# Performance work log

Measured on AMD Instinct MI355X. Metric: run time of the kernel, lower is better.

## Reference

```python
import jax, jax.numpy as jnp
import numpy as np

HIDDEN_DIM = 1024
SEQ_LEN = 4096
D_IN = 1024


def setup_inputs() -> dict:
    key = jax.random.key(0)
    ks = jax.random.split(key, 9)
    s = 1.0 / np.sqrt(D_IN)
    return {
        "q": jax.random.normal(ks[0], (SEQ_LEN, D_IN), jnp.float32),
        "k": jax.random.normal(ks[1], (SEQ_LEN, D_IN), jnp.float32),
        "v": jax.random.normal(ks[2], (SEQ_LEN, D_IN), jnp.float32),
        "Wq": jax.random.normal(ks[3], (D_IN, HIDDEN_DIM), jnp.float32) * s,
        "bq": jnp.zeros((HIDDEN_DIM,), jnp.float32),
        "Wk": jax.random.normal(ks[4], (D_IN, HIDDEN_DIM), jnp.float32) * s,
        "bk": jnp.zeros((HIDDEN_DIM,), jnp.float32),
        "Wv": jax.random.normal(ks[5], (D_IN, HIDDEN_DIM), jnp.float32) * s,
        "bv": jnpp_zeros() if False else jnp.zeros((HIDDEN_DIM,), jnp.float32),
    }


def reference(q, k, v, Wq, bq, Wk, bk, Wv, bv):
    # Dense projections (flax Dense: x @ W + b)
    query = q @ Wq + bq          # [S, H]
    key_p = k @ Wk + bk          # [S, H]
    value = v @ Wv + bv          # [S, H]
    # scores = Q K^T / sqrt(hidden_dim)  -> [S, S]
    scores = jnp.matmul(query, key_p.T) / jnp.sqrt(jnp.float32(HIDDEN_DIM))
    weights = jax.nn.softmax(scores, axis=-1)
    context = jnp.matmul(weights, value)  # [S, H]
    return context
```

## Files before the change

kernel.cpp:

```cpp
#include <hip/hip_runtime.h>


typedef short short4v __attribute__((ext_vector_type(4)));
typedef short short8  __attribute__((ext_vector_type(8)));
typedef float f32x4   __attribute__((ext_vector_type(4)));

#define MFMA16 __builtin_amdgcn_mfma_f32_16x16x32_bf16

__device__ __forceinline__ short f2bf(float f) {
    union { float f; unsigned u; } x; x.f = f;
    unsigned r = (x.u + 0x7FFFu + ((x.u >> 16) & 1u)) >> 16;
    return (short)r;
}
__device__ __forceinline__ float bf2f(short s) {
    union { unsigned u; float f; } x;
    x.u = ((unsigned)(unsigned short)s) << 16; return x.f;
}
__device__ __forceinline__ void store_out(short* p, float v) { *p = f2bf(v); }
__device__ __forceinline__ void store_out(float* p, float v) { *p = v; }

__device__ __forceinline__ void gl2lds(const short* g, short* l) {
    __builtin_amdgcn_global_load_lds(
        (const __attribute__((address_space(1))) void*)g,
        (__attribute__((address_space(3))) void*)l, 16, 0, 0);
}

__global__ __launch_bounds__(256) void prep_w(
    const float* __restrict__ W0, const float* __restrict__ W1,
    const float* __restrict__ W2, short* __restrict__ Wt)
{
    __shared__ float tile[64][65];
    const float* W = blockIdx.z == 0 ? W0 : (blockIdx.z == 1 ? W1 : W2);
    short* T = Wt + (size_t)blockIdx.z * 1048576;
    const int c0 = blockIdx.x * 64;
    const int r0 = blockIdx.y * 64;
    const int tx = threadIdx.x & 63;
    const int ty = threadIdx.x >> 6;
    #pragma unroll
    for (int p = 0; p < 16; ++p) {
        int r = ty + p * 4;
        tile[r][tx] = W[(size_t)(r0 + r) * 1024 + c0 + tx];
    }
    __syncthreads();
    #pragma unroll
    for (int p = 0; p < 16; ++p) {
        int r = ty + p * 4;
        T[(size_t)(c0 + r) * 1024 + r0 + tx] = f2bf(tile[tx][r]);
    }
}

__global__ __launch_bounds__(256) void cast_qkv(
    const float* __restrict__ q, const float* __restrict__ k,
    const float* __restrict__ v, short* __restrict__ xb)
{
    const float* src = blockIdx.z == 0 ? q : (blockIdx.z == 1 ? k : v);
    short* dst = xb + (size_t)blockIdx.z * 4194304;
    for (int i = blockIdx.x * 256 + threadIdx.x; i < 1048576; i += 256 * 1024) {
        float4 f = ((const float4*)src)[i];
        short4v o;
        o[0] = f2bf(f.x); o[1] = f2bf(f.y); o[2] = f2bf(f.z); o[3] = f2bf(f.w);
        ((short4v*)dst)[i] = o;
    }
}

__global__ __launch_bounds__(256) void transpose_v(
    const short* __restrict__ src, short* __restrict__ dst)
{
    __shared__ short t[64][65];
    const int c0 = blockIdx.x * 64;
    const int r0 = blockIdx.y * 64;
    const int tx = threadIdx.x & 63;
    const int ty = threadIdx.x >> 6;
    #pragma unroll
    for (int p = 0; p < 16; ++p) {
        const int r = p * 4 + ty;
        t[r][tx] = src[(size_t)(r0 + r) * 1024 + c0 + tx];
    }
    __syncthreads();
    #pragma unroll
    for (int p = 0; p < 16; ++p) {
        const int r = p * 4 + ty;
        dst[(size_t)(c0 + r) * 4096 + r0 + tx] = t[tx][r];
    }
}

template <typename TOut, int MODE>
__global__ __launch_bounds__(512, 4) void gemm128(
    const short* __restrict__ A, const short* __restrict__ Bt,
    const float* __restrict__ b0, const float* __restrict__ b1,
    const float* __restrict__ b2,
    TOut* __restrict__ C, float* __restrict__ P1, float* __restrict__ P2,
    float* __restrict__ P3,
    int M, int N, int lda, int ldb, float scale,
    int nc, int nc_last, int kstep)
{
    __shared__ short Lds[24576];

    const int t    = threadIdx.x;
    const int lane = t & 63;
    const int wv   = t >> 6;

    const int nb  = gridDim.x;
    const int bid = blockIdx.y * nb + blockIdx.x;
    const int band   = bid / (8 * nb);
    const int within = bid - band * 8 * nb;
    const int m0 = (band * 8 + (within & 7)) * 128;
    const int n0 = (within >> 3) * 256;

    const float* bias = nullptr;
    int kbeg = 0;
    TOut* Cw = C;
    if constexpr (MODE == 1) {
        const int z = blockIdx.z;
        A  += (size_t)z * M * lda;
        Bt += (size_t)z * N * ldb;
        Cw  = C + (size_t)z * M * N;
        bias = z == 0 ? b0 : (z == 1 ? b1 : b2);
    }
    if constexpr (MODE == 2) {
        const int z = blockIdx.z;
        kbeg = z * kstep;
        if (z == (int)gridDim.z - 1) nc = nc_last;
        Cw = (TOut*)(z == 0 ? (float*)C : (z == 1 ? P1 : (z == 2 ? P2 : P3)));
    }
    (void)b0; (void)b1; (void)b2; (void)P1; (void)P2; (void)P3;
    (void)nc_last; (void)kstep;

    const int srow = lane >> 2;
    const int skof = ((lane & 3) ^ ((lane >> 3) & 3)) * 8;
    const short* pA  = A  + (size_t)(m0 + wv * 16 + srow) * lda + kbeg + skof;
    const short* pB0 = Bt + (size_t)(n0 + wv * 16 + srow) * ldb + kbeg + skof;
    const short* pB1 = pB0 + (size_t)128 * ldb;
    short* sA  = Lds + wv * 512;
    short* sB0 = Lds + 4096 + wv * 512;
    short* sB1 = Lds + 8192 + wv * 512;

    const int wm = wv >> 2, wn = wv & 3;
    const int lr = lane & 15, lq = lane >> 4;
    const int pcol = lq ^ ((lr >> 1) & 3);
    const short* rdA = Lds + (wm * 64 + lr) * 32 + pcol * 8;
    const short* rdB = Lds + 4096 + (wn * 64 + lr) * 32 + pcol * 8;

    f32x4 acc[4][4];
    #pragma unroll
    for (int i = 0; i < 4; ++i)
        #pragma unroll
        for (int j = 0; j < 4; ++j) { f32x4 z4 = {0.f,0.f,0.f,0.f}; acc[i][j] = z4; }

#define STAGE(c) {                                                        \
    const int s_ = (c) & 1;                                               \
    const size_t ko_ = (size_t)(c) * 32;                                  \
    gl2lds(pA  + ko_, sA  + s_ * 12288);                                  \
    gl2lds(pB0 + ko_, sB0 + s_ * 12288);                                  \
    gl2lds(pB1 + ko_, sB1 + s_ * 12288); }

#define COMPUTE(c) {                                                      \
    const short* rA_ = rdA + ((c) & 1) * 12288;                           \
    const short* rB_ = rdB + ((c) & 1) * 12288;                           \
    short8 af[4], bf_[4];                                                 \
    _Pragma("unroll") for (int i = 0; i < 4; ++i)                         \
        af[i] = *(const short8*)(rA_ + i * 512);                          \
    _Pragma("unroll") for (int j = 0; j < 4; ++j)                         \
        bf_[j] = *(const short8*)(rB_ + j * 512);                         \
    __builtin_amdgcn_s_setprio(1);                                        \
    _Pragma("unroll") for (int i = 0; i < 4; ++i)                         \
        _Pragma("unroll") for (int j = 0; j < 4; ++j)                     \
            acc[i][j] = MFMA16(af[i], bf_[j], acc[i][j], 0, 0, 0);        \
    __builtin_amdgcn_s_setprio(0); }

    STAGE(0);

    for (int c = 0; c < nc - 1; ++c) {
        STAGE(c + 1);
        asm volatile("s_waitcnt vmcnt(3)" ::: "memory");
        __builtin_amdgcn_s_barrier();
        COMPUTE(c);
        __builtin_amdgcn_s_barrier();
    }
    asm volatile("s_waitcnt vmcnt(0)" ::: "memory");
    __builtin_amdgcn_s_barrier();
    COMPUTE(nc - 1);
#undef COMPUTE
#undef STAGE

    #pragma unroll
    for (int i = 0; i < 4; ++i) {
        const int crow = m0 + wm * 64 + i * 16 + lq * 4;
        #pragma unroll
        for (int j = 0; j < 4; ++j) {
            const int ccol = n0 + wn * 64 + j * 16 + lr;
            float bb = 0.f;
            if constexpr (MODE == 1) bb = bias[ccol];
            #pragma unroll
            for (int r = 0; r < 4; ++r) {
                float val = acc[i][j][r] * scale + bb;
                store_out(&Cw[(size_t)(crow + r) * N + ccol], val);
            }
        }
    }
}

__global__ __launch_bounds__(256) void softmax_bf16(short* __restrict__ S)
{
    const int row = blockIdx.x;
    short8* r8 = (short8*)(S + (size_t)row * 4096);
    const int t = threadIdx.x;

    float x[16];
    #pragma unroll
    for (int i = 0; i < 2; ++i) {
        short8 raw = r8[t + 256 * i];
        #pragma unroll
        for (int j = 0; j < 8; ++j) x[8 * i + j] = bf2f(raw[j]);
    }
    float m = -1e30f;
    #pragma unroll
    for (int i = 0; i < 16; ++i) m = fmaxf(m, x[i]);
    #pragma unroll
    for (int off = 32; off > 0; off >>= 1) m = fmaxf(m, __shfl_xor(m, off));

    __shared__ float redm[4], reds[4];
    const int wv = t >> 6;
    if ((t & 63) == 0) redm[wv] = m;
    __syncthreads();
    m = fmaxf(fmaxf(redm[0], redm[1]), fmaxf(redm[2], redm[3]));

    float s = 0.f;
    #pragma unroll
    for (int i = 0; i < 16; ++i) { x[i] = __expf(x[i] - m); s += x[i]; }
    #pragma unroll
    for (int off = 32; off > 0; off >>= 1) s += __shfl_xor(s, off);
    if ((t & 63) == 0) reds[wv] = s;
    __syncthreads();
    s = reds[0] + reds[1] + reds[2] + reds[3];
    const float inv = 1.f / s;

    #pragma unroll
    for (int i = 0; i < 2; ++i) {
        short8 o;
        #pragma unroll
        for (int j = 0; j < 8; ++j) o[j] = f2bf(x[8 * i + j] * inv);
        r8[t + 256 * i] = o;
    }
}

__global__ __launch_bounds__(256) void combine(
    float* __restrict__ out, const float* __restrict__ a,
    const float* __restrict__ b, const float* __restrict__ c, int np)
{
    for (int i = blockIdx.x * 256 + threadIdx.x; i < 1048576; i += 256 * 1024) {
        float4 o = ((const float4*)out)[i];
        float4 x = ((const float4*)a)[i];
        float4 y = ((const float4*)b)[i];
        o.x += x.x + y.x; o.y += x.y + y.y;
        o.z += x.z + y.z; o.w += x.w + y.w;
        if (np == 3) {
            float4 w = ((const float4*)c)[i];
            o.x += w.x; o.y += w.y; o.z += w.z; o.w += w.w;
        }
        ((float4*)out)[i] = o;
    }
}

extern "C" void kernel_launch(void* const* d_in, const int* in_sizes, int n_in,
                              void* d_out, int out_size, void* d_ws, size_t ws_size,
                              hipStream_t stream)
{
    const float* q  = (const float*)d_in[0];
    const float* k  = (const float*)d_in[1];
    const float* v  = (const float*)d_in[2];
    const float* Wq = (const float*)d_in[3];
    const float* bq = (const float*)d_in[4];
    const float* Wk = (const float*)d_in[5];
    const float* bk = (const float*)d_in[6];
    const float* Wv = (const float*)d_in[7];
    const float* bv = (const float*)d_in[8];
    float* out = (float*)d_out;

    char* ws = (char*)d_ws;
    const size_t MB = 1ull << 20;
    short* Wt = (short*)(ws + 0);
    short* xb = (short*)(ws + 6 * MB);
    short* pr = (short*)(ws + 30 * MB);
    short* S  = (short*)(ws + 46 * MB);
    short* Vt = (short*)(ws + 78 * MB);
    float* p1 = (float*)(ws + 0);
    float* p2 = (float*)(ws + 16 * MB);
    float* p3 = (float*)(ws + 86 * MB);
    const int SK = (ws_size >= 102 * MB) ? 4 : 3;

    prep_w<<<dim3(16, 16, 3), 256, 0, stream>>>(Wq, Wk, Wv, Wt);
    cast_qkv<<<dim3(1024, 1, 3), 256, 0, stream>>>(q, k, v, xb);
    gemm128<short, 1><<<dim3(4, 32, 3), 512, 0, stream>>>(
        xb, Wt, bq, bk, bv, pr, nullptr, nullptr, nullptr,
        4096, 1024, 1024, 1024, 1.f, 32, 32, 0);
    transpose_v<<<dim3(16, 64), 256, 0, stream>>>(pr + 8 * 1024 * 1024, Vt);
    gemm128<short, 0><<<dim3(16, 32), 512, 0, stream>>>(
        pr, pr + 4 * 1024 * 1024, nullptr, nullptr, nullptr, S,
        nullptr, nullptr, nullptr,
        4096, 4096, 1024, 1024, 0.03125f, 32, 32, 0);
    softmax_bf16<<<4096, 256, 0, stream>>>(S);
    if (SK == 4) {
        gemm128<float, 2><<<dim3(4, 32, 4), 512, 0, stream>>>(
            S, Vt, nullptr, nullptr, nullptr, out, p1, p2, p3,
            4096, 1024, 4096, 4096, 1.f, 32, 32, 1024);
        combine<<<1024, 256, 0, stream>>>(out, p1, p2, p3, 3);
    } else {
        gemm128<float, 2><<<dim3(4, 32, 3), 512, 0, stream>>>(
            S, Vt, nullptr, nullptr, nullptr, out, p1, p2, nullptr,
            4096, 1024, 4096, 4096, 1.f, 42, 44, 1344);
        combine<<<1024, 256, 0, stream>>>(out, p1, p2, nullptr, 2);
    }
}
```

Before: 254.2 us.

## Fuse V transpose into projection GEMM epilogue and shrink GEMM tile to 128x128

Removes the separate transpose_v kernel: the V-projection blocks write their bf16 output transposed directly into Vt through LDS staging in the epilogue. All GEMMs switch from 512-thread 128x256 tiles to 256-thread 128x128 tiles with doubled grids. This is meant to cut one launch and one round trip of V through memory, and to improve load balance across CUs. The cost is lower data reuse per block and an extra LDS pass in the V epilogue.

```diff
diff --git a/kernel.cpp b/kernel.cpp
--- a/kernel.cpp
+++ b/kernel.cpp
@@ -63,38 +63,17 @@
     }
 }
 
-__global__ __launch_bounds__(256) void transpose_v(
-    const short* __restrict__ src, short* __restrict__ dst)
-{
-    __shared__ short t[64][65];
-    const int c0 = blockIdx.x * 64;
-    const int r0 = blockIdx.y * 64;
-    const int tx = threadIdx.x & 63;
-    const int ty = threadIdx.x >> 6;
-    #pragma unroll
-    for (int p = 0; p < 16; ++p) {
-        const int r = p * 4 + ty;
-        t[r][tx] = src[(size_t)(r0 + r) * 1024 + c0 + tx];
-    }
-    __syncthreads();
-    #pragma unroll
-    for (int p = 0; p < 16; ++p) {
-        const int r = p * 4 + ty;
-        dst[(size_t)(c0 + r) * 4096 + r0 + tx] = t[tx][r];
-    }
-}
-
 template <typename TOut, int MODE>
-__global__ __launch_bounds__(512, 4) void gemm128(
+__global__ __launch_bounds__(256, 4) void gemm128(
     const short* __restrict__ A, const short* __restrict__ Bt,
     const float* __restrict__ b0, const float* __restrict__ b1,
     const float* __restrict__ b2,
     TOut* __restrict__ C, float* __restrict__ P1, float* __restrict__ P2,
-    float* __restrict__ P3,
+    float* __restrict__ P3, short* __restrict__ Vt,
     int M, int N, int lda, int ldb, float scale,
     int nc, int nc_last, int kstep)
 {
-    __shared__ short Lds[24576];
+    __shared__ short Lds[16384];
 
     const int t    = threadIdx.x;
     const int lane = t & 63;
@@ -105,7 +84,7 @@
     const int band   = bid / (8 * nb);
     const int within = bid - band * 8 * nb;
     const int m0 = (band * 8 + (within & 7)) * 128;
-    const int n0 = (within >> 3) * 256;
+    const int n0 = (within >> 3) * 128;
 
     const float* bias = nullptr;
     int kbeg = 0;
@@ -123,19 +102,21 @@
         if (z == (int)gridDim.z - 1) nc = nc_last;
         Cw = (TOut*)(z == 0 ? (float*)C : (z == 1 ? P1 : (z == 2 ? P2 : P3)));
     }
-    (void)b0; (void)b1; (void)b2; (void)P1; (void)P2; (void)P3;
+    (void)b0; (void)b1; (void)b2; (void)P1; (void)P2; (void)P3; (void)Vt;
     (void)nc_last; (void)kstep;
 
     const int srow = lane >> 2;
     const int skof = ((lane & 3) ^ ((lane >> 3) & 3)) * 8;
-    const short* pA  = A  + (size_t)(m0 + wv * 16 + srow) * lda + kbeg + skof;
-    const short* pB0 = Bt + (size_t)(n0 + wv * 16 + srow) * ldb + kbeg + skof;
-    const short* pB1 = pB0 + (size_t)128 * ldb;
-    short* sA  = Lds + wv * 512;
-    short* sB0 = Lds + 4096 + wv * 512;
-    short* sB1 = Lds + 8192 + wv * 512;
-
-    const int wm = wv >> 2, wn = wv & 3;
+    const short* pA0 = A  + (size_t)(m0 + wv * 32 + srow) * lda + kbeg + skof;
+    const short* pA1 = pA0 + (size_t)16 * lda;
+    const short* pB0 = Bt + (size_t)(n0 + wv * 32 + srow) * ldb + kbeg + skof;
+    const short* pB1 = pB0 + (size_t)16 * ldb;
+    short* sA0 = Lds + wv * 1024;
+    short* sA1 = sA0 + 512;
+    short* sB0 = Lds + 4096 + wv * 1024;
+    short* sB1 = sB0 + 512;
+
+    const int wm = wv >> 1, wn = wv & 1;
     const int lr = lane & 15, lq = lane >> 4;
     const int pcol = lq ^ ((lr >> 1) & 3);
     const short* rdA = Lds + (wm * 64 + lr) * 32 + pcol * 8;
@@ -150,13 +131,14 @@
 #define STAGE(c) {                                                        \
     const int s_ = (c) & 1;                                               \
     const size_t ko_ = (size_t)(c) * 32;                                  \
-    gl2lds(pA  + ko_, sA  + s_ * 12288);                                  \
-    gl2lds(pB0 + ko_, sB0 + s_ * 12288);                                  \
-    gl2lds(pB1 + ko_, sB1 + s_ * 12288); }
+    gl2lds(pA0 + ko_, sA0 + s_ * 8192);                                   \
+    gl2lds(pA1 + ko_, sA1 + s_ * 8192);                                   \
+    gl2lds(pB0 + ko_, sB0 + s_ * 8192);                                   \
+    gl2lds(pB1 + ko_, sB1 + s_ * 8192); }
 
 #define COMPUTE(c) {                                                      \
-    const short* rA_ = rdA + ((c) & 1) * 12288;                           \
-    const short* rB_ = rdB + ((c) & 1) * 12288;                           \
+    const short* rA_ = rdA + ((c) & 1) * 8192;                            \
+    const short* rB_ = rdB + ((c) & 1) * 8192;                            \
     short8 af[4], bf_[4];                                                 \
     _Pragma("unroll") for (int i = 0; i < 4; ++i)                         \
         af[i] = *(const short8*)(rA_ + i * 512);                          \
@@ -172,7 +154,7 @@
 
     for (int c = 0; c < nc - 1; ++c) {
         STAGE(c + 1);
-        asm volatile("s_waitcnt vmcnt(3)" ::: "memory");
+        asm volatile("s_waitcnt vmcnt(4)" ::: "memory");
         __builtin_amdgcn_s_barrier();
         COMPUTE(c);
         __builtin_amdgcn_s_barrier();
@@ -183,6 +165,39 @@
 #undef COMPUTE
 #undef STAGE
 
+    if constexpr (MODE == 1) {
+        if (blockIdx.z == 2) {
+            #pragma unroll
+            for (int hh = 0; hh < 2; ++hh) {
+                __syncthreads();
+                if (wn == hh) {
+                    #pragma unroll
+                    for (int i = 0; i < 4; ++i) {
+                        #pragma unroll
+                        for (int j = 0; j < 4; ++j) {
+                            const int colL = wn * 64 + j * 16 + lr;
+                            const float bb = bias[n0 + colL];
+                            #pragma unroll
+                            for (int r = 0; r < 4; ++r) {
+                                const int rowL = wm * 64 + i * 16 + lq * 4 + r;
+                                Lds[(colL - 64 * hh) * 136 + rowL] =
+                                    f2bf(acc[i][j][r] * scale + bb);
+                            }
+                        }
+                    }
+                }
+                __syncthreads();
+                const int c = t >> 2, part = t & 3;
+                short* dst = Vt + (size_t)(n0 + 64 * hh + c) * 4096
+                                + m0 + part * 32;
+                const short* src = &Lds[c * 136 + part * 32];
+                #pragma unroll
+                for (int s = 0; s < 4; ++s)
+                    ((short8*)dst)[s] = ((const short8*)src)[s];
+            }
+            return;
+        }
+    }
     #pragma unroll
     for (int i = 0; i < 4; ++i) {
         const int crow = m0 + wm * 64 + i * 16 + lq * 4;
@@ -291,23 +306,22 @@
 
     prep_w<<<dim3(16, 16, 3), 256, 0, stream>>>(Wq, Wk, Wv, Wt);
     cast_qkv<<<dim3(1024, 1, 3), 256, 0, stream>>>(q, k, v, xb);
-    gemm128<short, 1><<<dim3(4, 32, 3), 512, 0, stream>>>(
-        xb, Wt, bq, bk, bv, pr, nullptr, nullptr, nullptr,
+    gemm128<short, 1><<<dim3(8, 32, 3), 256, 0, stream>>>(
+        xb, Wt, bq, bk, bv, pr, nullptr, nullptr, nullptr, Vt,
         4096, 1024, 1024, 1024, 1.f, 32, 32, 0);
-    transpose_v<<<dim3(16, 64), 256, 0, stream>>>(pr + 8 * 1024 * 1024, Vt);
-    gemm128<short, 0><<<dim3(16, 32), 512, 0, stream>>>(
+    gemm128<short, 0><<<dim3(32, 32), 256, 0, stream>>>(
         pr, pr + 4 * 1024 * 1024, nullptr, nullptr, nullptr, S,
-        nullptr, nullptr, nullptr,
+        nullptr, nullptr, nullptr, nullptr,
         4096, 4096, 1024, 1024, 0.03125f, 32, 32, 0);
     softmax_bf16<<<4096, 256, 0, stream>>>(S);
     if (SK == 4) {
-        gemm128<float, 2><<<dim3(4, 32, 4), 512, 0, stream>>>(
-            S, Vt, nullptr, nullptr, nullptr, out, p1, p2, p3,
+        gemm128<float, 2><<<dim3(8, 32, 4), 256, 0, stream>>>(
+            S, Vt, nullptr, nullptr, nullptr, out, p1, p2, p3, nullptr,
             4096, 1024, 4096, 4096, 1.f, 32, 32, 1024);
         combine<<<1024, 256, 0, stream>>>(out, p1, p2, p3, 3);
     } else {
-        gemm128<float, 2><<<dim3(4, 32, 3), 512, 0, stream>>>(
-            S, Vt, nullptr, nullptr, nullptr, out, p1, p2, nullptr,
+        gemm128<float, 2><<<dim3(8, 32, 3), 256, 0, stream>>>(
+            S, Vt, nullptr, nullptr, nullptr, out, p1, p2, nullptr, nullptr,
             4096, 1024, 4096, 4096, 1.f, 42, 44, 1344);
         combine<<<1024, 256, 0, stream>>>(out, p1, p2, nullptr, 2);
     }
```

Measured after the change: 263.0 us. 1.03x slower.

## Fuse V transpose into projection GEMM epilogue and stage bf16 stores through LDS

Applied to the files above, without the earlier changes.

The projection GEMM's V slice now writes its output transposed directly into Vt through an LDS staging tile, which removes the separate transpose_v kernel and its extra pass over V. The bf16 epilogues for the projection and QK^T GEMMs also stage tiles in LDS so each thread writes 16-byte vectors, replacing scattered 2-byte stores. The cost is extra barriers and LDS traffic in the epilogue, plus reuse of the GEMM's LDS buffer after the main loop.

```diff
diff --git a/kernel.cpp b/kernel.cpp
--- a/kernel.cpp
+++ b/kernel.cpp
@@ -16,8 +16,6 @@
     union { unsigned u; float f; } x;
     x.u = ((unsigned)(unsigned short)s) << 16; return x.f;
 }
-__device__ __forceinline__ void store_out(short* p, float v) { *p = f2bf(v); }
-__device__ __forceinline__ void store_out(float* p, float v) { *p = v; }
 
 __device__ __forceinline__ void gl2lds(const short* g, short* l) {
     __builtin_amdgcn_global_load_lds(
@@ -63,34 +61,13 @@
     }
 }
 
-__global__ __launch_bounds__(256) void transpose_v(
-    const short* __restrict__ src, short* __restrict__ dst)
-{
-    __shared__ short t[64][65];
-    const int c0 = blockIdx.x * 64;
-    const int r0 = blockIdx.y * 64;
-    const int tx = threadIdx.x & 63;
-    const int ty = threadIdx.x >> 6;
-    #pragma unroll
-    for (int p = 0; p < 16; ++p) {
-        const int r = p * 4 + ty;
-        t[r][tx] = src[(size_t)(r0 + r) * 1024 + c0 + tx];
-    }
-    __syncthreads();
-    #pragma unroll
-    for (int p = 0; p < 16; ++p) {
-        const int r = p * 4 + ty;
-        dst[(size_t)(c0 + r) * 4096 + r0 + tx] = t[tx][r];
-    }
-}
-
 template <typename TOut, int MODE>
 __global__ __launch_bounds__(512, 4) void gemm128(
     const short* __restrict__ A, const short* __restrict__ Bt,
     const float* __restrict__ b0, const float* __restrict__ b1,
     const float* __restrict__ b2,
     TOut* __restrict__ C, float* __restrict__ P1, float* __restrict__ P2,
-    float* __restrict__ P3,
+    float* __restrict__ P3, short* __restrict__ Vt,
     int M, int N, int lda, int ldb, float scale,
     int nc, int nc_last, int kstep)
 {
@@ -114,7 +91,7 @@
         const int z = blockIdx.z;
         A  += (size_t)z * M * lda;
         Bt += (size_t)z * N * ldb;
-        Cw  = C + (size_t)z * M * N;
+        Cw  = C + (size_t)(z < 2 ? z : 0) * M * N;
         bias = z == 0 ? b0 : (z == 1 ? b1 : b2);
     }
     if constexpr (MODE == 2) {
@@ -123,7 +100,7 @@
         if (z == (int)gridDim.z - 1) nc = nc_last;
         Cw = (TOut*)(z == 0 ? (float*)C : (z == 1 ? P1 : (z == 2 ? P2 : P3)));
     }
-    (void)b0; (void)b1; (void)b2; (void)P1; (void)P2; (void)P3;
+    (void)b0; (void)b1; (void)b2; (void)P1; (void)P2; (void)P3; (void)Vt;
     (void)nc_last; (void)kstep;
 
     const int srow = lane >> 2;
@@ -183,19 +160,81 @@
 #undef COMPUTE
 #undef STAGE
 
+    if constexpr (MODE == 1) {
+        if (blockIdx.z == 2) {
+            #pragma unroll
+            for (int hh = 0; hh < 4; ++hh) {
+                __syncthreads();
+                if (wn == hh) {
+                    #pragma unroll
+                    for (int i = 0; i < 4; ++i) {
+                        #pragma unroll
+                        for (int j = 0; j < 4; ++j) {
+                            const int colL = j * 16 + lr;
+                            const float bb = bias[n0 + hh * 64 + colL];
+                            #pragma unroll
+                            for (int r = 0; r < 4; ++r) {
+                                const int rowL = wm * 64 + i * 16 + lq * 4 + r;
+                                Lds[colL * 136 + rowL] =
+                                    f2bf(acc[i][j][r] * scale + bb);
+                            }
+                        }
+                    }
+                }
+                __syncthreads();
+                const int c = t >> 3, part = t & 7;
+                short* dst = Vt + (size_t)(n0 + hh * 64 + c) * 4096
+                                + m0 + part * 16;
+                const short* src = &Lds[c * 136 + part * 16];
+                *(short8*)dst       = *(const short8*)src;
+                *(short8*)(dst + 8) = *(const short8*)(src + 8);
+            }
+            return;
+        }
+    }
+
+    if constexpr (sizeof(TOut) == 2) {
+        #pragma unroll
+        for (int p = 0; p < 2; ++p) {
+            __syncthreads();
+            if (wm == p) {
+                #pragma unroll
+                for (int i = 0; i < 4; ++i) {
+                    #pragma unroll
+                    for (int j = 0; j < 4; ++j) {
+                        const int col = wn * 64 + j * 16 + lr;
+                        float bb = 0.f;
+                        if constexpr (MODE == 1) bb = bias[n0 + col];
+                        #pragma unroll
+                        for (int r = 0; r < 4; ++r) {
+                            const int row = i * 16 + lq * 4 + r;
+                            Lds[row * 272 + col] =
+                                f2bf(acc[i][j][r] * scale + bb);
+                        }
+                    }
+                }
+            }
+            __syncthreads();
+            const int row = t >> 3, part = t & 7;
+            short* dst = (short*)Cw + (size_t)(m0 + p * 64 + row) * N
+                          + n0 + part * 32;
+            const short* src = &Lds[row * 272 + part * 32];
+            #pragma unroll
+            for (int s = 0; s < 4; ++s)
+                ((short8*)dst)[s] = ((const short8*)src)[s];
+        }
+        return;
+    }
+
     #pragma unroll
     for (int i = 0; i < 4; ++i) {
         const int crow = m0 + wm * 64 + i * 16 + lq * 4;
         #pragma unroll
         for (int j = 0; j < 4; ++j) {
             const int ccol = n0 + wn * 64 + j * 16 + lr;
-            float bb = 0.f;
-            if constexpr (MODE == 1) bb = bias[ccol];
             #pragma unroll
-            for (int r = 0; r < 4; ++r) {
-                float val = acc[i][j][r] * scale + bb;
-                store_out(&Cw[(size_t)(crow + r) * N + ccol], val);
-            }
+            for (int r = 0; r < 4; ++r)
+                Cw[(size_t)(crow + r) * N + ccol] = acc[i][j][r] * scale;
         }
     }
 }
@@ -292,22 +331,21 @@
     prep_w<<<dim3(16, 16, 3), 256, 0, stream>>>(Wq, Wk, Wv, Wt);
     cast_qkv<<<dim3(1024, 1, 3), 256, 0, stream>>>(q, k, v, xb);
     gemm128<short, 1><<<dim3(4, 32, 3), 512, 0, stream>>>(
-        xb, Wt, bq, bk, bv, pr, nullptr, nullptr, nullptr,
+        xb, Wt, bq, bk, bv, pr, nullptr, nullptr, nullptr, Vt,
         4096, 1024, 1024, 1024, 1.f, 32, 32, 0);
-    transpose_v<<<dim3(16, 64), 256, 0, stream>>>(pr + 8 * 1024 * 1024, Vt);
     gemm128<short, 0><<<dim3(16, 32), 512, 0, stream>>>(
         pr, pr + 4 * 1024 * 1024, nullptr, nullptr, nullptr, S,
-        nullptr, nullptr, nullptr,
+        nullptr, nullptr, nullptr, nullptr,
         4096, 4096, 1024, 1024, 0.03125f, 32, 32, 0);
     softmax_bf16<<<4096, 256, 0, stream>>>(S);
     if (SK == 4) {
         gemm128<float, 2><<<dim3(4, 32, 4), 512, 0, stream>>>(
-            S, Vt, nullptr, nullptr, nullptr, out, p1, p2, p3,
+            S, Vt, nullptr, nullptr, nullptr, out, p1, p2, p3, nullptr,
             4096, 1024, 4096, 4096, 1.f, 32, 32, 1024);
         combine<<<1024, 256, 0, stream>>>(out, p1, p2, p3, 3);
     } else {
         gemm128<float, 2><<<dim3(4, 32, 3), 512, 0, stream>>>(
-            S, Vt, nullptr, nullptr, nullptr, out, p1, p2, nullptr,
+            S, Vt, nullptr, nullptr, nullptr, out, p1, p2, nullptr, nullptr,
             4096, 1024, 4096, 4096, 1.f, 42, 44, 1344);
         combine<<<1024, 256, 0, stream>>>(out, p1, p2, nullptr, 2);
     }
```

New measurement: 262.8 us. 1.03x slower.
